# Kernel optimization log

Measured on AMD Instinct MI355X. Metric: run time of the kernel, lower is better.

The kernel has to match this reference:

```python
import jax, jax.numpy as jnp
import numpy as np

N = 100000        # nodes
E = 3200000       # edges (avg degree 32)
IN_F = 128
OUT_F = 64
ALPHA = 0.2       # LeakyReLU negative slope
EPS = 1e-5        # LayerNorm eps


def setup_inputs() -> dict:
    key = jax.random.key(0)
    k = jax.random.split(key, 5)
    x = jax.random.normal(k[0], (N, IN_F), jnp.float32)
    edge = jax.random.randint(k[1], (2, E), 0, N, dtype=jnp.int32)
    # kaiming-normal inits as in the torch module
    W = jax.random.normal(k[2], (OUT_F, IN_F), jnp.float32) * np.float32(np.sqrt(2.0 / IN_F))
    b = jnp.zeros((OUT_F,), jnp.float32)
    a = jax.random.normal(k[3], (2 * OUT_F,), jnp.float32) * np.float32(np.sqrt(2.0 / (2 * OUT_F)))
    gamma = jnp.ones((OUT_F,), jnp.float32)
    beta = jnp.zeros((OUT_F,), jnp.float32)
    return {"x": x, "edge": edge, "W": W, "b": b, "a": a, "gamma": gamma, "beta": beta}


def reference(x, edge, W, b, a, gamma, beta):
    # h = Linear(in->out)
    h = x @ W.T + b                                   # [N, OUT_F]
    src, dst = edge[0], edge[1]
    # edge score a · cat(h[src], h[dst]) == (h @ a_l)[src] + (h @ a_r)[dst]
    sl = h @ a[:OUT_F]                                # [N]
    sr = h @ a[OUT_F:]                                # [N]
    score = sl[src] + sr[dst]                         # [E]
    lrelu = jnp.where(score > 0, score, ALPHA * score)
    edge_e = jnp.exp(-lrelu)                          # [E] (dropout=0 / eval)
    # sparse spmm: h_prime[i] = sum_{e: src_e==i} edge_e * h[dst_e]
    msg = edge_e[:, None] * h[dst]                    # [E, OUT_F]
    h_prime = jax.ops.segment_sum(msg, src, num_segments=N)  # [N, OUT_F]
    # LayerNorm over feature dim (biased variance, as torch)
    mu = jnp.mean(h_prime, axis=-1, keepdims=True)
    var = jnp.mean(jnp.square(h_prime - mu), axis=-1, keepdims=True)
    h_norm = (h_prime - mu) * jax.lax.rsqrt(var + EPS) * gamma + beta
    # concat=True -> ELU
    return jax.nn.elu(h_norm)
```

## Files before the change

kernel.cpp:

```cpp
#include <hip/hip_runtime.h>
#include <hip/hip_fp16.h>
#include <cstdint>
#include <cstddef>

#define INF_  128
#define OUTF  64
#define ALPHA 0.2f
#define LN_EPS 1e-5f

#define PBLK  256
#define NP2   784
#define NPS   1024
#define TILE  8192
#define HCAP  3072
#define PCNTMAX 4608
#define MAXK  9

typedef __attribute__((ext_vector_type(8))) _Float16 half8;
typedef __attribute__((ext_vector_type(4))) float    f32x4;

__global__ __launch_bounds__(256) void gemm_kernel(
    const float* __restrict__ x, const float* __restrict__ W,
    const float* __restrict__ b, const float* __restrict__ a,
    __half* __restrict__ hh, float* __restrict__ sl, float* __restrict__ sr, int n)
{
    __shared__ half8 wfrag_lds[16][64];

    const int tid  = threadIdx.x;
    const int lane = tid & 63;
    const int wv   = tid >> 6;
    const int col  = lane & 15;
    const int quad = lane >> 4;

    for (int idx = tid; idx < 1024; idx += 256) {
        const int l  = idx & 63, ct = idx >> 6;
        const int c  = ct >> 2,  t  = ct & 3;
        const int row = 4 * (l & 15) + t;
        const int k0  = 32 * c + 8 * (l >> 4);
        const float4 f0 = ((const float4*)W)[row * 32 + (k0 >> 2)];
        const float4 f1 = ((const float4*)W)[row * 32 + (k0 >> 2) + 1];
        half8 h;
        h[0] = (_Float16)f0.x; h[1] = (_Float16)f0.y;
        h[2] = (_Float16)f0.z; h[3] = (_Float16)f0.w;
        h[4] = (_Float16)f1.x; h[5] = (_Float16)f1.y;
        h[6] = (_Float16)f1.z; h[7] = (_Float16)f1.w;
        wfrag_lds[ct][l] = h;
    }
    __syncthreads();

    half8 bf[4][4];
    #pragma unroll
    for (int c = 0; c < 4; c++)
        #pragma unroll
        for (int t = 0; t < 4; t++)
            bf[c][t] = wfrag_lds[c * 4 + t][lane];

    const float4 b4  = ((const float4*)b)[col];
    const float4 al4 = ((const float4*)a)[col];
    const float4 ar4 = ((const float4*)a)[16 + col];

    const int ntile  = (n + 15) >> 4;
    const int wgid   = blockIdx.x * 4 + wv;
    const int nwaves = gridDim.x * 4;

    for (int tile = wgid; tile < ntile; tile += nwaves) {
        const int node0 = tile << 4;
        const int xr    = min(node0 + col, n - 1);
        const float* xrow = x + (size_t)xr * INF_ + 8 * quad;

        f32x4 acc0 = {0,0,0,0}, acc1 = {0,0,0,0}, acc2 = {0,0,0,0}, acc3 = {0,0,0,0};
        #pragma unroll
        for (int c = 0; c < 4; c++) {
            const float4 f0 = *(const float4*)(xrow + 32 * c);
            const float4 f1 = *(const float4*)(xrow + 32 * c + 4);
            half8 af;
            af[0] = (_Float16)f0.x; af[1] = (_Float16)f0.y;
            af[2] = (_Float16)f0.z; af[3] = (_Float16)f0.w;
            af[4] = (_Float16)f1.x; af[5] = (_Float16)f1.y;
            af[6] = (_Float16)f1.z; af[7] = (_Float16)f1.w;
            acc0 = __builtin_amdgcn_mfma_f32_16x16x32_f16(af, bf[c][0], acc0, 0, 0, 0);
            acc1 = __builtin_amdgcn_mfma_f32_16x16x32_f16(af, bf[c][1], acc1, 0, 0, 0);
            acc2 = __builtin_amdgcn_mfma_f32_16x16x32_f16(af, bf[c][2], acc2, 0, 0, 0);
            acc3 = __builtin_amdgcn_mfma_f32_16x16x32_f16(af, bf[c][3], acc3, 0, 0, 0);
        }

        #pragma unroll
        for (int reg = 0; reg < 4; reg++) {
            const int node = node0 + quad * 4 + reg;
            const float v0 = acc0[reg] + b4.x;
            const float v1 = acc1[reg] + b4.y;
            const float v2 = acc2[reg] + b4.z;
            const float v3 = acc3[reg] + b4.w;
            float p = v0 * al4.x + v1 * al4.y + v2 * al4.z + v3 * al4.w;
            float q = v0 * ar4.x + v1 * ar4.y + v2 * ar4.z + v3 * ar4.w;
            p += __shfl_xor(p, 1); p += __shfl_xor(p, 2);
            p += __shfl_xor(p, 4); p += __shfl_xor(p, 8);
            q += __shfl_xor(q, 1); q += __shfl_xor(q, 2);
            q += __shfl_xor(q, 4); q += __shfl_xor(q, 8);
            if (node < n) {
                ushort4 u;
                u.x = __half_as_ushort(__float2half(v0));
                u.y = __half_as_ushort(__float2half(v1));
                u.z = __half_as_ushort(__float2half(v2));
                u.w = __half_as_ushort(__float2half(v3));
                ((ushort4*)hh)[(size_t)node * 16 + col] = u;
                if (col == 0) { sl[node] = p; sr[node] = q; }
            }
        }
    }
}

__global__ __launch_bounds__(512) void count_kernel(
    const int* __restrict__ src, int* __restrict__ M, int E)
{
    __shared__ int hist[NPS];
    const int t = threadIdx.x;
    const int b = blockIdx.x;
    for (int i = t; i < NPS; i += 512) hist[i] = 0;
    __syncthreads();
    const int chunk = (E + PBLK - 1) / PBLK;
    const int lo = b * chunk;
    const int hi = min(E, lo + chunk);
    for (int e = lo + t; e < hi; e += 512)
        atomicAdd(&hist[src[e] >> 7], 1);
    __syncthreads();
    for (int p = t; p < NP2; p += 512)
        M[(size_t)p * PBLK + b] = hist[p];
}

__global__ __launch_bounds__(256) void rowscan_kernel(
    int* __restrict__ M, int* __restrict__ rowsum)
{
    __shared__ int ws[4];
    const int p    = blockIdx.x;
    const int t    = threadIdx.x;
    const int lane = t & 63;
    const int wv   = t >> 6;
    const int v = M[(size_t)p * PBLK + t];
    int s = v;
    #pragma unroll
    for (int d = 1; d < 64; d <<= 1) {
        const int u = __shfl(s, lane - d);
        if (lane >= d) s += u;
    }
    if (lane == 63) ws[wv] = s;
    __syncthreads();
    int cross = 0;
    #pragma unroll
    for (int w = 0; w < 4; w++)
        if (w < wv) cross += ws[w];
    M[(size_t)p * PBLK + t] = cross + s - v;
    if (t == PBLK - 1) rowsum[p] = cross + s;
}

__global__ __launch_bounds__(1024) void pbase_kernel(
    const int* __restrict__ rowsum, int* __restrict__ pbase)
{
    __shared__ int part[NPS];
    const int t = threadIdx.x;
    const int v = (t < NP2) ? rowsum[t] : 0;
    part[t] = v;
    __syncthreads();
    for (int d = 1; d < NPS; d <<= 1) {
        const int u = (t >= d) ? part[t - d] : 0;
        __syncthreads();
        part[t] += u;
        __syncthreads();
    }
    if (t < NP2) pbase[t] = part[t] - v;
    if (t == NP2 - 1) pbase[NP2] = part[t];
}

__global__ __launch_bounds__(1024) void part_scatter(
    const int* __restrict__ src, const int* __restrict__ dst,
    const int* __restrict__ M, const int* __restrict__ pbase,
    int* __restrict__ pk, int E)
{
    __shared__ int hist[NPS];
    __shared__ int bnd[NPS + 1];
    __shared__ int cur[NPS];
    __shared__ int gbase[NP2];
    __shared__ int buf[TILE];
    __shared__ unsigned char pbuf[TILE];
    __shared__ int wsum[16];
    __shared__ int wbase[16];

    const int t    = threadIdx.x;
    const int b    = blockIdx.x;
    const int lane = t & 63;
    const int wv   = t >> 6;

    for (int p = t; p < NP2; p += 1024)
        gbase[p] = pbase[p] + M[(size_t)p * PBLK + b];

    const int chunk = (E + PBLK - 1) / PBLK;
    const int lo = b * chunk;
    const int hi = min(E, lo + chunk);

    for (int tb = lo; tb < hi; tb += TILE) {
        const int tcnt = min(TILE, hi - tb);
        hist[t] = 0;
        __syncthreads();

        int pp[8], pay[8];
        #pragma unroll
        for (int k = 0; k < 8; k++) {
            const int e = tb + t + k * 1024;
            pp[k] = -1;
            if (e < hi) {
                const int s = src[e];
                pp[k]  = s >> 7;
                pay[k] = ((s & 127) << 17) | dst[e];
                atomicAdd(&hist[pp[k]], 1);
            }
        }
        __syncthreads();

        const int v = hist[t];
        int s = v;
        #pragma unroll
        for (int d = 1; d < 64; d <<= 1) {
            const int u = __shfl(s, lane - d);
            if (lane >= d) s += u;
        }
        if (lane == 63) wsum[wv] = s;
        __syncthreads();
        if (t < 16) {
            const int xv = wsum[t];
            int sc = xv;
            #pragma unroll
            for (int d = 1; d < 16; d <<= 1) {
                const int u = __shfl(sc, t - d);
                if (t >= d) sc += u;
            }
            wbase[t] = sc - xv;
        }
        __syncthreads();
        {
            const int eb = wbase[wv] + s - v;
            bnd[t] = eb;
            cur[t] = eb;
            if (t == 1023) bnd[1024] = eb + v;
        }
        __syncthreads();

        #pragma unroll
        for (int k = 0; k < 8; k++) {
            if (pp[k] >= 0) {
                const int r = atomicAdd(&cur[pp[k]], 1);
                buf[r]  = pay[k];
                pbuf[r] = (unsigned char)(pp[k] & 255);
            }
        }
        __syncthreads();

        const int c1 = bnd[256], c2_ = bnd[512], c3 = bnd[768];
        for (int idx = t; idx < tcnt; idx += 1024) {
            const int phi = (idx >= c1) + (idx >= c2_) + (idx >= c3);
            const int p   = (phi << 8) | (int)pbuf[idx];
            pk[gbase[p] + (idx - bnd[p])] = buf[idx];
        }
        __syncthreads();

        for (int p = t; p < NP2; p += 1024) gbase[p] += bnd[p + 1] - bnd[p];
        __syncthreads();
    }
}

__global__ __launch_bounds__(512) void gat_fused(
    const int* __restrict__ pk, const int* __restrict__ pbase,
    const float* __restrict__ sl, const float* __restrict__ sr,
    const __half* __restrict__ hh,
    const float* __restrict__ gamma, const float* __restrict__ beta,
    float* __restrict__ out, int n)
{
    __shared__ int    ldst[HCAP];
    __shared__ __half lwgt[HCAP];
    __shared__ float  lsl[64];
    __shared__ int    lhist[64];
    __shared__ int    lbase[65];

    const int Bh    = blockIdx.x;
    const int P     = Bh >> 1;
    const int hb    = Bh & 1;
    const int t     = threadIdx.x;
    const int lane  = t & 63;
    const int wv    = t >> 6;
    const int fgrp  = lane & 15;
    const int equad = lane >> 4;

    if (t < 64) {
        lhist[t] = 0;
        const int g = (P << 7) + (hb << 6) + t;
        lsl[t] = (g < n) ? sl[g] : 0.f;
    }
    const int p0  = pbase[P];
    const int cnt = min(pbase[P + 1] - p0, PCNTMAX);
    __syncthreads();

    const int myn = (cnt > t) ? (cnt - t + 511) >> 9 : 0;
    int   pkr[MAXK];
    float wf[MAXK];
    int   rk[MAXK];
    #pragma unroll
    for (int k = 0; k < MAXK; k++) {
        rk[k] = -1;
        if (k < myn) {
            const int v  = pk[p0 + t + (k << 9)];
            const int s7 = (v >> 17) & 127;
            if ((s7 >> 6) == hb) {
                pkr[k] = v;
                const int s6 = s7 & 63;
                rk[k] = atomicAdd(&lhist[s6], 1);
                const float sc = lsl[s6] + sr[v & 0x1FFFF];
                const float lr = sc > 0.f ? sc : ALPHA * sc;
                wf[k] = __expf(-lr);
            }
        }
    }
    __syncthreads();

    if (wv == 0) {
        const int v = lhist[lane];
        int s = v;
        #pragma unroll
        for (int d = 1; d < 64; d <<= 1) {
            const int u = __shfl(s, lane - d);
            if (lane >= d) s += u;
        }
        lbase[lane] = s - v;
        if (lane == 63) lbase[64] = s;
    }
    __syncthreads();

    #pragma unroll
    for (int k = 0; k < MAXK; k++) {
        if (rk[k] >= 0) {
            const int v = pkr[k];
            const int s6 = (v >> 17) & 63;
            const int p  = lbase[s6] + rk[k];
            if (p < HCAP) {
                ldst[p] = v & 0x1FFFF;
                lwgt[p] = __float2half(wf[k]);
            }
        }
    }
    __syncthreads();

    const float4 gm4 = ((const float4*)gamma)[fgrp];
    const float4 bt4 = ((const float4*)beta)[fgrp];

    for (int k = wv; k < 64; k += 8) {
        const int node = (P << 7) + (hb << 6) + k;
        const int nb   = min(lbase[k], HCAP);
        const int ne   = min(lbase[k + 1], HCAP);
        const int len  = ne - nb;

        float4 acc = make_float4(0.f, 0.f, 0.f, 0.f);

        const int e0 = equad, e1 = 4 + equad;
        int dA = 0, dB = 0; float wA = 0.f, wB = 0.f;
        if (e0 < len) { dA = ldst[nb + e0]; wA = __half2float(lwgt[nb + e0]); }
        if (e1 < len) { dB = ldst[nb + e1]; wB = __half2float(lwgt[nb + e1]); }
        uint2 uA = ((const uint2*)hh)[(size_t)dA * 16 + fgrp];
        uint2 uB = ((const uint2*)hh)[(size_t)dB * 16 + fgrp];

        for (int tt = 0; tt < len; tt += 8) {
            uint2 nA = make_uint2(0u, 0u), nB = make_uint2(0u, 0u);
            float nwA = 0.f, nwB = 0.f;
            if (tt + 8 < len) {
                const int f0 = tt + 8 + equad, f1 = tt + 12 + equad;
                int xA = 0, xB = 0;
                if (f0 < len) { xA = ldst[nb + f0]; nwA = __half2float(lwgt[nb + f0]); }
                if (f1 < len) { xB = ldst[nb + f1]; nwB = __half2float(lwgt[nb + f1]); }
                nA = ((const uint2*)hh)[(size_t)xA * 16 + fgrp];
                nB = ((const uint2*)hh)[(size_t)xB * 16 + fgrp];
            }
            const float2 fA0 = __half22float2(*(const __half2*)&uA.x);
            const float2 fA1 = __half22float2(*(const __half2*)&uA.y);
            const float2 fB0 = __half22float2(*(const __half2*)&uB.x);
            const float2 fB1 = __half22float2(*(const __half2*)&uB.y);
            acc.x = fmaf(wA, fA0.x, acc.x); acc.y = fmaf(wA, fA0.y, acc.y);
            acc.z = fmaf(wA, fA1.x, acc.z); acc.w = fmaf(wA, fA1.y, acc.w);
            acc.x = fmaf(wB, fB0.x, acc.x); acc.y = fmaf(wB, fB0.y, acc.y);
            acc.z = fmaf(wB, fB1.x, acc.z); acc.w = fmaf(wB, fB1.y, acc.w);
            uA = nA; uB = nB; wA = nwA; wB = nwB;
        }

        acc.x += __shfl_xor(acc.x, 16); acc.x += __shfl_xor(acc.x, 32);
        acc.y += __shfl_xor(acc.y, 16); acc.y += __shfl_xor(acc.y, 32);
        acc.z += __shfl_xor(acc.z, 16); acc.z += __shfl_xor(acc.z, 32);
        acc.w += __shfl_xor(acc.w, 16); acc.w += __shfl_xor(acc.w, 32);

        float s1 = acc.x + acc.y + acc.z + acc.w;
        float s2 = acc.x * acc.x + acc.y * acc.y + acc.z * acc.z + acc.w * acc.w;
        #pragma unroll
        for (int dd = 1; dd < 16; dd <<= 1) {
            s1 += __shfl_xor(s1, dd);
            s2 += __shfl_xor(s2, dd);
        }
        const float mu  = s1 * (1.f / 64.f);
        const float var = fmaxf(s2 * (1.f / 64.f) - mu * mu, 0.f);
        const float rs  = rsqrtf(var + LN_EPS);

        float4 y;
        y.x = (acc.x - mu) * rs * gm4.x + bt4.x;
        y.y = (acc.y - mu) * rs * gm4.y + bt4.y;
        y.z = (acc.z - mu) * rs * gm4.z + bt4.z;
        y.w = (acc.w - mu) * rs * gm4.w + bt4.w;
        y.x = y.x > 0.f ? y.x : __expf(y.x) - 1.f;
        y.y = y.y > 0.f ? y.y : __expf(y.y) - 1.f;
        y.z = y.z > 0.f ? y.z : __expf(y.z) - 1.f;
        y.w = y.w > 0.f ? y.w : __expf(y.w) - 1.f;
        if (node < n && equad == 0)
            ((float4*)out)[(size_t)node * 16 + fgrp] = y;
    }
}

extern "C" void kernel_launch(void* const* d_in, const int* in_sizes, int n_in,
                              void* d_out, int out_size, void* d_ws, size_t ws_size,
                              hipStream_t stream)
{
    const float* x     = (const float*)d_in[0];
    const int*   edge  = (const int*)  d_in[1];
    const float* W     = (const float*)d_in[2];
    const float* b     = (const float*)d_in[3];
    const float* a     = (const float*)d_in[4];
    const float* gamma = (const float*)d_in[5];
    const float* beta  = (const float*)d_in[6];
    float* out = (float*)d_out;

    const int n = in_sizes[0] / INF_;
    const int E = in_sizes[1] / 2;
    const int* src = edge;
    const int* dst = edge + E;
    const int npart = (n + 127) >> 7;
    const int nhalf = npart * 2;

    char* ws = (char*)d_ws;
    size_t offb = 0;
    auto alloc = [&](size_t bytes) -> void* {
        void* p = ws + offb;
        offb = (offb + bytes + 255) & ~(size_t)255;
        return p;
    };
    __half* hh     = (__half*)alloc((size_t)n * OUTF * 2);
    float*  sl     = (float*) alloc((size_t)n * 4);
    float*  sr     = (float*) alloc((size_t)n * 4);
    int*    M      = (int*)   alloc((size_t)NP2 * PBLK * 4);
    int*    rowsum = (int*)   alloc((size_t)NP2 * 4);
    int*    pbase  = (int*)   alloc((size_t)(NP2 + 1) * 4);
    int*    pk     = (int*)   alloc((size_t)E * 4);

    hipLaunchKernelGGL(count_kernel,   dim3(PBLK),  dim3(512),  0, stream, src, M, E);
    hipLaunchKernelGGL(rowscan_kernel, dim3(NP2),   dim3(256),  0, stream, M, rowsum);
    hipLaunchKernelGGL(pbase_kernel,   dim3(1),     dim3(1024), 0, stream, rowsum, pbase);
    hipLaunchKernelGGL(gemm_kernel,    dim3(1024),  dim3(256),  0, stream, x, W, b, a, hh, sl, sr, n);
    hipLaunchKernelGGL(part_scatter,   dim3(PBLK),  dim3(1024), 0, stream, src, dst, M, pbase, pk, E);
    hipLaunchKernelGGL(gat_fused,      dim3(nhalf), dim3(512),  0, stream, pk, pbase, sl, sr, hh, gamma, beta, out, n);
}
```

Baseline: 235.8 us.

## Replace count/scan partition pipeline with atomic slot reservation into fixed-capacity buckets

```diff
diff --git a/kernel.cpp b/kernel.cpp
--- a/kernel.cpp
+++ b/kernel.cpp
@@ -12,8 +12,8 @@
 #define NP2   784
 #define NPS   1024
 #define TILE  8192
+#define CAP   4608
 #define HCAP  3072
-#define PCNTMAX 4608
 #define MAXK  9
 
 typedef __attribute__((ext_vector_type(8))) _Float16 half8;
@@ -110,71 +110,9 @@
     }
 }
 
-__global__ __launch_bounds__(512) void count_kernel(
-    const int* __restrict__ src, int* __restrict__ M, int E)
-{
-    __shared__ int hist[NPS];
-    const int t = threadIdx.x;
-    const int b = blockIdx.x;
-    for (int i = t; i < NPS; i += 512) hist[i] = 0;
-    __syncthreads();
-    const int chunk = (E + PBLK - 1) / PBLK;
-    const int lo = b * chunk;
-    const int hi = min(E, lo + chunk);
-    for (int e = lo + t; e < hi; e += 512)
-        atomicAdd(&hist[src[e] >> 7], 1);
-    __syncthreads();
-    for (int p = t; p < NP2; p += 512)
-        M[(size_t)p * PBLK + b] = hist[p];
-}
-
-__global__ __launch_bounds__(256) void rowscan_kernel(
-    int* __restrict__ M, int* __restrict__ rowsum)
-{
-    __shared__ int ws[4];
-    const int p    = blockIdx.x;
-    const int t    = threadIdx.x;
-    const int lane = t & 63;
-    const int wv   = t >> 6;
-    const int v = M[(size_t)p * PBLK + t];
-    int s = v;
-    #pragma unroll
-    for (int d = 1; d < 64; d <<= 1) {
-        const int u = __shfl(s, lane - d);
-        if (lane >= d) s += u;
-    }
-    if (lane == 63) ws[wv] = s;
-    __syncthreads();
-    int cross = 0;
-    #pragma unroll
-    for (int w = 0; w < 4; w++)
-        if (w < wv) cross += ws[w];
-    M[(size_t)p * PBLK + t] = cross + s - v;
-    if (t == PBLK - 1) rowsum[p] = cross + s;
-}
-
-__global__ __launch_bounds__(1024) void pbase_kernel(
-    const int* __restrict__ rowsum, int* __restrict__ pbase)
-{
-    __shared__ int part[NPS];
-    const int t = threadIdx.x;
-    const int v = (t < NP2) ? rowsum[t] : 0;
-    part[t] = v;
-    __syncthreads();
-    for (int d = 1; d < NPS; d <<= 1) {
-        const int u = (t >= d) ? part[t - d] : 0;
-        __syncthreads();
-        part[t] += u;
-        __syncthreads();
-    }
-    if (t < NP2) pbase[t] = part[t] - v;
-    if (t == NP2 - 1) pbase[NP2] = part[t];
-}
-
 __global__ __launch_bounds__(1024) void part_scatter(
     const int* __restrict__ src, const int* __restrict__ dst,
-    const int* __restrict__ M, const int* __restrict__ pbase,
-    int* __restrict__ pk, int E)
+    int* __restrict__ gcnt, int* __restrict__ pk, int E)
 {
     __shared__ int hist[NPS];
     __shared__ int bnd[NPS + 1];
@@ -190,9 +128,6 @@
     const int lane = t & 63;
     const int wv   = t >> 6;
 
-    for (int p = t; p < NP2; p += 1024)
-        gbase[p] = pbase[p] + M[(size_t)p * PBLK + b];
-
     const int chunk = (E + PBLK - 1) / PBLK;
     const int lo = b * chunk;
     const int hi = min(E, lo + chunk);
@@ -244,6 +179,12 @@
         }
         __syncthreads();
 
+        if (t < NP2) {
+            const int c = bnd[t + 1] - bnd[t];
+            gbase[t] = c ? atomicAdd(&gcnt[t], c) : 0;
+        }
+        __syncthreads();
+
         #pragma unroll
         for (int k = 0; k < 8; k++) {
             if (pp[k] >= 0) {
@@ -258,17 +199,16 @@
         for (int idx = t; idx < tcnt; idx += 1024) {
             const int phi = (idx >= c1) + (idx >= c2_) + (idx >= c3);
             const int p   = (phi << 8) | (int)pbuf[idx];
-            pk[gbase[p] + (idx - bnd[p])] = buf[idx];
-        }
-        __syncthreads();
-
-        for (int p = t; p < NP2; p += 1024) gbase[p] += bnd[p + 1] - bnd[p];
+            const int off = gbase[p] + (idx - bnd[p]);
+            if (off < CAP)
+                pk[(size_t)p * CAP + off] = buf[idx];
+        }
         __syncthreads();
     }
 }
 
 __global__ __launch_bounds__(512) void gat_fused(
-    const int* __restrict__ pk, const int* __restrict__ pbase,
+    const int* __restrict__ pk, const int* __restrict__ gcnt,
     const float* __restrict__ sl, const float* __restrict__ sr,
     const __half* __restrict__ hh,
     const float* __restrict__ gamma, const float* __restrict__ beta,
@@ -294,8 +234,8 @@
         const int g = (P << 7) + (hb << 6) + t;
         lsl[t] = (g < n) ? sl[g] : 0.f;
     }
-    const int p0  = pbase[P];
-    const int cnt = min(pbase[P + 1] - p0, PCNTMAX);
+    const int cnt = min(gcnt[P], CAP);
+    const size_t p0 = (size_t)P * CAP;
     __syncthreads();
 
     const int myn = (cnt > t) ? (cnt - t + 511) >> 9 : 0;
@@ -436,6 +376,8 @@
     const int* dst = edge + E;
     const int npart = (n + 127) >> 7;
     const int nhalf = npart * 2;
+    const int ntile = (n + 15) >> 4;
+    const int gemmg = (ntile + 3) >> 2;
 
     char* ws = (char*)d_ws;
     size_t offb = 0;
@@ -444,18 +386,14 @@
         offb = (offb + bytes + 255) & ~(size_t)255;
         return p;
     };
-    __half* hh     = (__half*)alloc((size_t)n * OUTF * 2);
-    float*  sl     = (float*) alloc((size_t)n * 4);
-    float*  sr     = (float*) alloc((size_t)n * 4);
-    int*    M      = (int*)   alloc((size_t)NP2 * PBLK * 4);
-    int*    rowsum = (int*)   alloc((size_t)NP2 * 4);
-    int*    pbase  = (int*)   alloc((size_t)(NP2 + 1) * 4);
-    int*    pk     = (int*)   alloc((size_t)E * 4);
-
-    hipLaunchKernelGGL(count_kernel,   dim3(PBLK),  dim3(512),  0, stream, src, M, E);
-    hipLaunchKernelGGL(rowscan_kernel, dim3(NP2),   dim3(256),  0, stream, M, rowsum);
-    hipLaunchKernelGGL(pbase_kernel,   dim3(1),     dim3(1024), 0, stream, rowsum, pbase);
-    hipLaunchKernelGGL(gemm_kernel,    dim3(1024),  dim3(256),  0, stream, x, W, b, a, hh, sl, sr, n);
-    hipLaunchKernelGGL(part_scatter,   dim3(PBLK),  dim3(1024), 0, stream, src, dst, M, pbase, pk, E);
-    hipLaunchKernelGGL(gat_fused,      dim3(nhalf), dim3(512),  0, stream, pk, pbase, sl, sr, hh, gamma, beta, out, n);
+    __half* hh   = (__half*)alloc((size_t)n * OUTF * 2);
+    float*  sl   = (float*) alloc((size_t)n * 4);
+    float*  sr   = (float*) alloc((size_t)n * 4);
+    int*    gcnt = (int*)   alloc((size_t)NP2 * 4);
+    int*    pk   = (int*)   alloc((size_t)NP2 * CAP * 4);
+
+    hipMemsetAsync(gcnt, 0, (size_t)NP2 * 4, stream);
+    hipLaunchKernelGGL(part_scatter, dim3(PBLK),  dim3(1024), 0, stream, src, dst, gcnt, pk, E);
+    hipLaunchKernelGGL(gemm_kernel,  dim3(gemmg), dim3(256),  0, stream, x, W, b, a, hh, sl, sr, n);
+    hipLaunchKernelGGL(gat_fused,    dim3(nhalf), dim3(512),  0, stream, pk, gcnt, sl, sr, hh, gamma, beta, out, n);
 }
```

Measured after the change: 226.1 us. 1.04x faster.
